# Kernel tuning notes

Hardware: AMD Instinct MI355X
Metric: run time of the kernel (lower is better)

The kernel has to match this reference:

```python
import jax, jax.numpy as jnp
import numpy as np

NUM_HEADS = 8
HEAD_SPLITS = [2, 3, 3]   # heads per conv window group (windows 3,5,7)


def _dwconv(x, w, b):
    # depthwise conv2d, SAME padding; x [B,Cg,H,W], w [Cg,1,k,k]
    k = w.shape[-1]
    pad = k // 2
    out = jax.lax.conv_general_dilated(
        x, w, window_strides=(1, 1), padding=[(pad, pad), (pad, pad)],
        feature_group_count=x.shape[1])
    return out + b[None, :, None, None]


def setup_inputs() -> dict:
    key = jax.random.key(0)
    ks = jax.random.split(key, 8)
    B, Hs, Ws, C = 16, 56, 56, 512
    N = 1 + Hs * Ws
    Ch = C // NUM_HEADS
    inp = {
        "x": jax.random.normal(ks[0], (B, N, C), dtype=jnp.float32),
        "qkv_w": jax.random.normal(ks[1], (3 * C, C), dtype=jnp.float32) * 0.02,
        "qkv_b": jnp.zeros((3 * C,), dtype=jnp.float32),
        "proj_w": jax.random.normal(ks[2], (C, C), dtype=jnp.float32) * 0.02,
        "proj_b": jnp.zeros((C,), dtype=jnp.float32),
        "conv_w3": jax.random.normal(ks[3], (2 * Ch, 1, 3, 3), dtype=jnp.float32) * 0.1,
        "conv_b3": jnp.zeros((2 * Ch,), dtype=jnp.float32),
        "conv_w5": jax.random.normal(ks[4], (3 * Ch, 1, 5, 5), dtype=jnp.float32) * 0.1,
        "conv_b5": jnp.zeros((3 * Ch,), dtype=jnp.float32),
        "conv_w7": jax.random.normal(ks[5], (3 * Ch, 1, 7, 7), dtype=jnp.float32) * 0.1,
        "conv_b7": jnp.zeros((3 * Ch,), dtype=jnp.float32),
        "H": 56,
        "W": 56,
    }
    return inp


def reference(x, qkv_w, qkv_b, proj_w, proj_b,
              conv_w3, conv_b3, conv_w5, conv_b5, conv_w7, conv_b7, H, W):
    B, N, C = x.shape
    h = NUM_HEADS
    Ch = C // h
    scale = Ch ** -0.5

    # qkv projection -> [3, B, h, N, Ch]
    qkv = (x @ qkv_w.T + qkv_b).reshape(B, N, 3, h, Ch)
    qkv = jnp.transpose(qkv, (2, 0, 3, 1, 4))
    q, k, v = qkv[0], qkv[1], qkv[2]

    # linear-attention factorization: softmax over tokens, then small Ch x Ch matmuls
    k_sm = jax.nn.softmax(k, axis=2)                     # softmax over N
    kv = jnp.einsum('bhnk,bhnd->bhkd', k_sm, v)          # [B,h,Ch,Ch]
    factor_att = jnp.einsum('bhnk,bhkd->bhnd', q, kv)    # [B,h,N,Ch]

    # conv relative-position encoding (CoaT ConvRelPosEnc)
    q_img = q[:, :, 1:, :]                               # drop CLS token
    v_img = v[:, :, 1:, :]
    v_img = jnp.transpose(v_img, (0, 1, 3, 2)).reshape(B, h * Ch, H, W)
    splits = np.cumsum([s * Ch for s in HEAD_SPLITS])[:-1]
    p3, p5, p7 = jnp.split(v_img, splits, axis=1)
    conv_v = jnp.concatenate([
        _dwconv(p3, conv_w3, conv_b3),
        _dwconv(p5, conv_w5, conv_b5),
        _dwconv(p7, conv_w7, conv_b7)], axis=1)           # [B,h*Ch,H,W]
    conv_v = jnp.transpose(conv_v.reshape(B, h, Ch, H * W), (0, 1, 3, 2))
    ev = q_img * conv_v                                   # [B,h,HW,Ch]
    crpe = jnp.concatenate(
        [jnp.zeros((B, h, 1, Ch), dtype=x.dtype), ev], axis=2)

    out = scale * factor_att + crpe                       # [B,h,N,Ch]
    out = jnp.transpose(out, (0, 2, 1, 3)).reshape(B, N, C)
    return out @ proj_w.T + proj_b
```

## Files before the change

### kernel.cpp

```cpp
#include <hip/hip_runtime.h>
#include <stdint.h>

#define NHEADS 8
#define NTOK   3137
#define BATCH  16
#define CDIM   512
#define MT     (BATCH*NTOK)

typedef unsigned short u16;
typedef float f32x4  __attribute__((ext_vector_type(4)));
typedef short bf16x8 __attribute__((ext_vector_type(8)));

__device__ __forceinline__ float bf2f(u16 u){
  union { uint32_t i; float f; } x; x.i = ((uint32_t)u) << 16; return x.f;
}
__device__ __forceinline__ u16 f2bf(float f){
  union { float f; uint32_t i; } x; x.f = f;
  uint32_t r = x.i + 0x7fffu + ((x.i >> 16) & 1u);
  return (u16)(r >> 16);
}
__device__ __forceinline__ void async_ld16(void* lds, const void* g){
  __builtin_amdgcn_global_load_lds((const __attribute__((address_space(1))) void*)g,
                                   (__attribute__((address_space(3))) void*)lds, 16, 0, 0);
}
#define BARM()   asm volatile("s_barrier" ::: "memory")
#define WAITV(N) asm volatile("s_waitcnt vmcnt(" #N ")" ::: "memory")
#define MFMA16(d,a,b) d = __builtin_amdgcn_mfma_f32_16x16x32_bf16(a,b,d,0,0,0)

__global__ void cvt_kernel(const float* __restrict__ src, u16* __restrict__ dst, int n4){
  int i = blockIdx.x * blockDim.x + threadIdx.x;
  if (i < n4){
    float4 v = ((const float4*)src)[i];
    uint32_t lo = ((uint32_t)f2bf(v.y) << 16) | f2bf(v.x);
    uint32_t hi = ((uint32_t)f2bf(v.w) << 16) | f2bf(v.z);
    ((uint2*)dst)[i] = make_uint2(lo, hi);
  }
}

template<int BM,int BN,int WM,int WN,int MODE>
__global__ __launch_bounds__(WM*WN*64, 2) void gemm2(
    const u16* __restrict__ A, const u16* __restrict__ Bw, const float* __restrict__ bias,
    u16* __restrict__ q_s, u16* __restrict__ k_s, u16* __restrict__ v_s,
    float* __restrict__ outF, int M)
{
  constexpr int THREADS = WM*WN*64;
  constexpr int MF = BM/(WM*16);
  constexpr int NF = BN/(WN*16);
  constexpr int WROWS = BM/WM;
  constexpr int WCOLS = BN/WN;
  static_assert((BM*8)/THREADS + (BN*8)/THREADS == 8, "vmcnt literal assumes 8 loads/stage");
  __shared__ __align__(16) u16 smem[2*(BM+BN)*64];

  const int t = threadIdx.x;
  const int w = t >> 6, l = t & 63;
  const int wr = w / WN, wc = w % WN;
  const int lr = l & 15, lg = l >> 4;

  const int nx = gridDim.x;
  const int nwg = nx * gridDim.y;
  const int orig = blockIdx.y * nx + blockIdx.x;
  const int q8 = nwg >> 3, r8 = nwg & 7;
  const int xcd = orig & 7;
  const int wgid = (xcd < r8 ? xcd*(q8+1) : r8*(q8+1) + (xcd-r8)*q8) + (orig >> 3);
  const int n0 = (wgid % nx) * BN;
  const int m0 = (wgid / nx) * BM;

  f32x4 acc[MF][NF];
#pragma unroll
  for (int i=0;i<MF;i++)
#pragma unroll
    for (int j=0;j<NF;j++) acc[i][j] = (f32x4){0.f,0.f,0.f,0.f};

  auto stage = [&](int bi, int k0){
    u16* da = smem + bi*(BM*64);
    u16* db = smem + 2*BM*64 + bi*(BN*64);
#pragma unroll
    for (int j=0;j<(BM*8)/THREADS;j++){
      int qc = t + THREADS*j;
      int R = qc >> 3, c = qc & 7;
      int cs = (c ^ (R & 7)) * 8;
      int ar = m0 + R; if (ar > M-1) ar = M-1;
      async_ld16(&da[qc*8], &A[(size_t)ar*512 + k0 + cs]);
    }
#pragma unroll
    for (int j=0;j<(BN*8)/THREADS;j++){
      int qc = t + THREADS*j;
      int R = qc >> 3, c = qc & 7;
      int cs = (c ^ (R & 7)) * 8;
      async_ld16(&db[qc*8], &Bw[(size_t)(n0+R)*512 + k0 + cs]);
    }
  };

  stage(0, 0);
  int cur = 0;
  for (int kt = 0; kt < 8; ++kt){
    if (kt < 7) stage(cur ^ 1, (kt+1)*64);
    if (kt < 7) { WAITV(8); } else { WAITV(0); }
    BARM();
    const u16* a_base = smem + cur*(BM*64);
    const u16* b_base = smem + 2*BM*64 + cur*(BN*64);
    __builtin_amdgcn_s_setprio(1);
#pragma unroll
    for (int ks=0; ks<2; ks++){
      bf16x8 af[MF], bfv[NF];
      int chunk = ks*4 + lg;
#pragma unroll
      for (int fi=0;fi<MF;fi++){
        int row = wr*WROWS + fi*16 + lr;
        af[fi] = *(const bf16x8*)&a_base[row*64 + ((chunk ^ (row & 7))*8)];
      }
#pragma unroll
      for (int fj=0;fj<NF;fj++){
        int col = wc*WCOLS + fj*16 + lr;
        bfv[fj] = *(const bf16x8*)&b_base[col*64 + ((chunk ^ (col & 7))*8)];
      }
#pragma unroll
      for (int fi=0;fi<MF;fi++)
#pragma unroll
        for (int fj=0;fj<NF;fj++)
          acc[fi][fj] = __builtin_amdgcn_mfma_f32_16x16x32_bf16(af[fi], bfv[fj], acc[fi][fj], 0, 0, 0);
    }
    __builtin_amdgcn_s_setprio(0);
    BARM();
    cur ^= 1;
  }

  if (MODE == 0){
    u16* warea = smem + w * (WROWS*WCOLS);
    float bvv[NF];
#pragma unroll
    for (int fj=0;fj<NF;fj++) bvv[fj] = bias[n0 + wc*WCOLS + fj*16 + lr];
#pragma unroll
    for (int fi=0;fi<MF;fi++)
#pragma unroll
      for (int fj=0;fj<NF;fj++)
#pragma unroll
        for (int r=0;r<4;r++)
          warea[(fi*16 + lg*4 + r)*WCOLS + fj*16 + lr] = f2bf(acc[fi][fj][r] + bvv[fj]);
    __syncthreads();
    const int colo = n0 + wc*WCOLS;
    const int part = colo >> 9;
    const int hq   = (colo >> 6) & 7;
    u16* dst = (part == 0) ? q_s : ((part == 1) ? k_s : v_s);
    const int rsub = l >> 3;
    const int csub = (l & 7) * 8;
#pragma unroll
    for (int pass=0; pass<WROWS/8; ++pass){
      int rl = pass*8 + rsub;
      int m = m0 + wr*WROWS + rl;
      if (m < M){
        int bb = m / NTOK;
        int n  = m - bb*NTOK;
        uint4 vv = *(const uint4*)&warea[rl*WCOLS + csub];
        *(uint4*)&dst[((size_t)(bb*8 + hq)*NTOK + n)*64 + csub] = vv;
      }
    }
  } else {
    float* warea = (float*)smem + w * (WROWS*WCOLS);
    float bvv[NF];
#pragma unroll
    for (int fj=0;fj<NF;fj++) bvv[fj] = bias[n0 + wc*WCOLS + fj*16 + lr];
#pragma unroll
    for (int fi=0;fi<MF;fi++)
#pragma unroll
      for (int fj=0;fj<NF;fj++)
#pragma unroll
        for (int r=0;r<4;r++)
          warea[(fi*16 + lg*4 + r)*WCOLS + fj*16 + lr] = acc[fi][fj][r] + bvv[fj];
    __syncthreads();
    const int colo = n0 + wc*WCOLS;
    const int rsub = l >> 4;
    const int csub = (l & 15) * 4;
#pragma unroll
    for (int pass=0; pass<WROWS/4; ++pass){
      int rl = pass*4 + rsub;
      int m = m0 + wr*WROWS + rl;
      if (m < M){
        float4 vv = *(const float4*)&warea[rl*WCOLS + csub];
        *(float4*)&outF[(size_t)m*512 + colo + csub] = vv;
      }
    }
  }
}

__global__ __launch_bounds__(256) void kv_partial(
    const u16* __restrict__ k_s, const u16* __restrict__ v_s,
    float* __restrict__ kv_p, float* __restrict__ s_p)
{
  __shared__ float smem[18432];
  const int t  = threadIdx.x;
  const int bh = blockIdx.x;
  const int hf = blockIdx.y;
  const size_t base = (size_t)bh * NTOK * 64;
  const int srow = t >> 3;
  const int scol = (t & 7) * 8;
  const int ns = t >> 6;
  const int kg = (t >> 3) & 7;
  const int dg = t & 7;

  float accv[8][8];
#pragma unroll
  for (int a=0;a<8;a++)
#pragma unroll
    for (int c=0;c<8;c++) accv[a][c] = 0.f;
  float s_loc[8];
#pragma unroll
  for (int i=0;i<8;i++) s_loc[i] = 0.f;

  float* ek = smem;
  float* vv = smem + 2048;
  const int n_beg = hf * 800;
  const int n_end = (hf == 3) ? NTOK : (n_beg + 800);

  for (int n0 = n_beg; n0 < n_end; n0 += 32){
    __syncthreads();
    int n = n0 + srow;
    float et[8], vf[8];
    if (n < n_end){
      uint4 kvec = *(const uint4*)&k_s[base + (size_t)n*64 + scol];
      uint4 vvec = *(const uint4*)&v_s[base + (size_t)n*64 + scol];
      const u16* kp = (const u16*)&kvec;
      const u16* vp = (const u16*)&vvec;
#pragma unroll
      for (int i=0;i<8;i++){
        et[i] = __expf(bf2f(kp[i]));
        s_loc[i] += et[i];
        vf[i] = bf2f(vp[i]);
      }
    } else {
#pragma unroll
      for (int i=0;i<8;i++){ et[i]=0.f; vf[i]=0.f; }
    }
    *(float4*)&ek[srow*64 + scol]     = make_float4(et[0],et[1],et[2],et[3]);
    *(float4*)&ek[srow*64 + scol + 4] = make_float4(et[4],et[5],et[6],et[7]);
    *(float4*)&vv[srow*64 + scol]     = make_float4(vf[0],vf[1],vf[2],vf[3]);
    *(float4*)&vv[srow*64 + scol + 4] = make_float4(vf[4],vf[5],vf[6],vf[7]);
    __syncthreads();
#pragma unroll
    for (int i=0;i<8;i++){
      int nl = ns + 4*i;
      float4 e0 = *(const float4*)&ek[nl*64 + kg*8];
      float4 e1 = *(const float4*)&ek[nl*64 + kg*8 + 4];
      float4 v0 = *(const float4*)&vv[nl*64 + dg*8];
      float4 v1 = *(const float4*)&vv[nl*64 + dg*8 + 4];
      float ea[8] = {e0.x,e0.y,e0.z,e0.w,e1.x,e1.y,e1.z,e1.w};
      float va[8] = {v0.x,v0.y,v0.z,v0.w,v1.x,v1.y,v1.z,v1.w};
#pragma unroll
      for (int a=0;a<8;a++)
#pragma unroll
        for (int c=0;c<8;c++) accv[a][c] += ea[a]*va[c];
    }
  }
  __syncthreads();
  float* part_kv = smem;
  float* part_s  = smem + 16384;
#pragma unroll
  for (int a=0;a<8;a++)
#pragma unroll
    for (int c=0;c<8;c++)
      part_kv[(size_t)ns*4096 + (kg*8+a)*64 + dg*8+c] = accv[a][c];
#pragma unroll
  for (int i=0;i<8;i++) part_s[srow*64 + scol + i] = s_loc[i];
  __syncthreads();
  const size_t obase = ((size_t)hf*128 + bh) * 4096;
  for (int i=0;i<16;i++){
    int e = t*16 + i;
    kv_p[obase + e] = part_kv[e] + part_kv[4096+e] + part_kv[8192+e] + part_kv[12288+e];
  }
  if (t < 64){
    float s = 0.f;
    for (int r=0;r<32;r++) s += part_s[r*64 + t];
    s_p[((size_t)hf*128 + bh)*64 + t] = s;
  }
}

__global__ void kv_reduce(const float* __restrict__ kv_p, const float* __restrict__ s_p,
                          u16* __restrict__ kvT){
  const int bh = blockIdx.x, t = threadIdx.x;
  for (int i=0;i<16;i++){
    int e = t*16 + i;
    int k = e >> 6, d = e & 63;
    float v = 0.f, S = 0.f;
#pragma unroll
    for (int hf=0; hf<4; hf++){
      v += kv_p[(size_t)(hf*128 + bh)*4096 + e];
      S += s_p[(hf*128 + bh)*64 + k];
    }
    kvT[(size_t)bh*4096 + d*64 + k] = f2bf(v / S);
  }
}

template<int R>
__global__ __launch_bounds__(256) void conv_fa(
    const u16* __restrict__ v_s, const u16* __restrict__ q_s,
    const u16* __restrict__ kvT,
    const float* __restrict__ wsrc, const float* __restrict__ bsrc,
    int h0, u16* __restrict__ out_pre)
{
  constexpr int KK = 2*R + 1;
  constexpr int TAPS = KK*KK;
  __shared__ __align__(16) u16 smem[8192 + KK*3584];
  u16* vt = smem + 8192;
  const int t = threadIdx.x;
  const int y  = blockIdx.x;
  const int hh = blockIdx.y;
  const int b  = blockIdx.z;
  const int h  = h0 + hh;
  const int bh = b*8 + h;
  const size_t base = (size_t)bh * NTOK * 64;
  const int n0 = 1 + y*56;

#pragma unroll
  for (int j=0;j<2;j++){
    int qq = t + 256*j;
    int row = qq >> 3, c = qq & 7;
    int cs = (c ^ (row & 7)) * 8;
    int n = n0 + row; if (n > NTOK-1) n = NTOK-1;
    async_ld16(&smem[qq*8], &q_s[base + (size_t)n*64 + cs]);
    async_ld16(&smem[4096 + qq*8], &kvT[(size_t)bh*4096 + row*64 + cs]);
  }
  for (int ry=0; ry<KK; ry++){
    int yy = y - R + ry;
    for (int idx = t; idx < 448; idx += 256){
      uint4 val = make_uint4(0u,0u,0u,0u);
      if (yy >= 0 && yy < 56)
        val = *(const uint4*)&v_s[base + (size_t)(1 + yy*56)*64 + idx*8];
      *(uint4*)&vt[ry*3584 + idx*8] = val;
    }
  }
  __syncthreads();

  const int w = t >> 6, l = t & 63;
  const int lr = l & 15, lg = l >> 4;
  f32x4 fac[4];
#pragma unroll
  for (int j=0;j<4;j++) fac[j] = (f32x4){0.f,0.f,0.f,0.f};
#pragma unroll
  for (int ks=0; ks<2; ks++){
    int chunk = ks*4 + lg;
    int arow = w*16 + lr;
    bf16x8 af = *(const bf16x8*)&smem[arow*64 + ((chunk ^ (arow & 7))*8)];
#pragma unroll
    for (int fj=0; fj<4; fj++){
      int col = fj*16 + lr;
      bf16x8 bvv = *(const bf16x8*)&smem[4096 + col*64 + ((chunk ^ (col & 7))*8)];
      MFMA16(fac[fj], af, bvv);
    }
  }

  const int d = l;
  const int xg = w;
  float wreg[TAPS];
#pragma unroll
  for (int i=0;i<TAPS;i++) wreg[i] = wsrc[(hh*64 + d)*TAPS + i];
  const float bias = bsrc[hh*64 + d];
  float creg[14];
#pragma unroll
  for (int i=0;i<14;i++) creg[i] = bias;
  const int x0 = xg * 14;
#pragma unroll
  for (int ry=0; ry<KK; ry++){
    float rw[14 + 2*R];
#pragma unroll
    for (int i=0; i<14+2*R; i++){
      int xx = x0 - R + i;
      rw[i] = (xx >= 0 && xx < 56) ? bf2f(vt[ry*3584 + xx*64 + d]) : 0.f;
    }
#pragma unroll
    for (int xi=0; xi<14; xi++)
#pragma unroll
      for (int rx=0; rx<KK; rx++)
        creg[xi] += rw[xi+rx] * wreg[ry*KK + rx];
  }

  float qv[14];
#pragma unroll
  for (int xi=0; xi<14; xi++){
    int row = x0 + xi;
    int chunk = d >> 3, e = d & 7;
    qv[xi] = bf2f(smem[row*64 + ((chunk ^ (row & 7))*8) + e]);
  }

  __syncthreads();
  float* fa = (float*)smem;
#pragma unroll
  for (int fj=0; fj<4; fj++)
#pragma unroll
    for (int r=0; r<4; r++)
      fa[(w*16 + lg*4 + r)*64 + fj*16 + lr] = 0.125f * fac[fj][r];
  __syncthreads();

#pragma unroll
  for (int xi=0; xi<14; xi++){
    int nn = n0 + x0 + xi;
    out_pre[((size_t)b*NTOK + nn)*CDIM + h*64 + d] =
        f2bf(fa[(x0 + xi)*64 + d] + creg[xi]*qv[xi]);
  }
}

__global__ void fa0_kernel(const u16* __restrict__ q_s, const u16* __restrict__ kvT,
                           u16* __restrict__ out_pre){
  const int b = blockIdx.x, t = threadIdx.x;
  const int h = t >> 6, d = t & 63;
  const int bh = b*8 + h;
  float s = 0.f;
#pragma unroll
  for (int k=0; k<64; k++)
    s += bf2f(q_s[(size_t)bh*NTOK*64 + k]) * bf2f(kvT[(size_t)bh*4096 + d*64 + k]);
  out_pre[(size_t)b*NTOK*CDIM + h*64 + d] = f2bf(0.125f * s);
}

extern "C" void kernel_launch(void* const* d_in, const int* in_sizes, int n_in,
                              void* d_out, int out_size, void* d_ws, size_t ws_size,
                              hipStream_t stream)
{
  const float* x      = (const float*)d_in[0];
  const float* qkv_w  = (const float*)d_in[1];
  const float* qkv_b  = (const float*)d_in[2];
  const float* proj_w = (const float*)d_in[3];
  const float* proj_b = (const float*)d_in[4];
  const float* w3 = (const float*)d_in[5];
  const float* b3 = (const float*)d_in[6];
  const float* w5 = (const float*)d_in[7];
  const float* b5 = (const float*)d_in[8];
  const float* w7 = (const float*)d_in[9];
  const float* b7 = (const float*)d_in[10];
  float* out = (float*)d_out;

  char* ws = (char*)d_ws;
  size_t off = 0;
  auto alloc = [&](size_t bytes) -> void* {
    void* p = ws + off;
    off += (bytes + 255) & ~(size_t)255;
    return p;
  };
  u16*   x_bf     = (u16*)alloc((size_t)MT*512*2);
  u16*   qkvw_bf  = (u16*)alloc((size_t)1536*512*2);
  u16*   projw_bf = (u16*)alloc((size_t)512*512*2);
  u16*   q_s      = (u16*)alloc((size_t)128*NTOK*64*2);
  u16*   k_s      = (u16*)alloc((size_t)128*NTOK*64*2);
  u16*   v_s      = (u16*)alloc((size_t)128*NTOK*64*2);
  u16*   kvT      = (u16*)alloc((size_t)128*4096*2);
  float* kv_p     = (float*)alloc((size_t)4*128*4096*4);
  float* s_p      = (float*)alloc((size_t)4*128*64*4);
  u16*   out_pre  = x_bf;

  { int n4 = (MT*512)/4;   cvt_kernel<<<(n4+255)/256, 256, 0, stream>>>(x, x_bf, n4); }
  { int n4 = (1536*512)/4; cvt_kernel<<<(n4+255)/256, 256, 0, stream>>>(qkv_w, qkvw_bf, n4); }
  { int n4 = (512*512)/4;  cvt_kernel<<<(n4+255)/256, 256, 0, stream>>>(proj_w, projw_bf, n4); }

  gemm2<256,256,2,4,0><<<dim3(6, 197), 512, 0, stream>>>(
      x_bf, qkvw_bf, qkv_b, q_s, k_s, v_s, nullptr, MT);

  kv_partial<<<dim3(128, 4), 256, 0, stream>>>(k_s, v_s, kv_p, s_p);
  kv_reduce<<<128, 256, 0, stream>>>(kv_p, s_p, kvT);
  fa0_kernel<<<16, 512, 0, stream>>>(q_s, kvT, out_pre);

  conv_fa<1><<<dim3(56, 2, 16), 256, 0, stream>>>(v_s, q_s, kvT, w3, b3, 0, out_pre);
  conv_fa<2><<<dim3(56, 3, 16), 256, 0, stream>>>(v_s, q_s, kvT, w5, b5, 2, out_pre);
  conv_fa<3><<<dim3(56, 3, 16), 256, 0, stream>>>(v_s, q_s, kvT, w7, b7, 5, out_pre);

  gemm2<128,128,2,2,1><<<dim3(4, 393), 256, 0, stream>>>(
      out_pre, projw_bf, proj_b, nullptr, nullptr, nullptr, out, MT);
}
```

Before: 383.9 us.

## Use MFMA for KV reduction and unify proj GEMM to 256x256 tiles

Replaces the scalar FP32 outer-product kv_partial kernel with an MFMA-based kernel that stores exp(k) and v transposed in bf16 shared memory with XOR swizzle. It also fixes the GEMM template to 256x256 tiles for both the QKV and output projections, splitting the fp32 epilogue into two halves to fit shared memory. The explicit vmcnt waits and raw barriers are replaced by __syncthreads. The intent is to cut the FP32 ALU cost of the kv reduction and use larger proj tiles, at the price of bf16 rounding of exp(k) and possibly weaker load/compute overlap in the GEMM loop.

```diff
diff --git a/kernel.cpp b/kernel.cpp
--- a/kernel.cpp
+++ b/kernel.cpp
@@ -23,8 +23,6 @@
   __builtin_amdgcn_global_load_lds((const __attribute__((address_space(1))) void*)g,
                                    (__attribute__((address_space(3))) void*)lds, 16, 0, 0);
 }
-#define BARM()   asm volatile("s_barrier" ::: "memory")
-#define WAITV(N) asm volatile("s_waitcnt vmcnt(" #N ")" ::: "memory")
 #define MFMA16(d,a,b) d = __builtin_amdgcn_mfma_f32_16x16x32_bf16(a,b,d,0,0,0)
 
 __global__ void cvt_kernel(const float* __restrict__ src, u16* __restrict__ dst, int n4){
@@ -37,18 +35,16 @@
   }
 }
 
-template<int BM,int BN,int WM,int WN,int MODE>
-__global__ __launch_bounds__(WM*WN*64, 2) void gemm2(
+template<int MODE>
+__global__ __launch_bounds__(512, 2) void gemm2(
     const u16* __restrict__ A, const u16* __restrict__ Bw, const float* __restrict__ bias,
     u16* __restrict__ q_s, u16* __restrict__ k_s, u16* __restrict__ v_s,
     float* __restrict__ outF, int M)
 {
-  constexpr int THREADS = WM*WN*64;
-  constexpr int MF = BM/(WM*16);
-  constexpr int NF = BN/(WN*16);
-  constexpr int WROWS = BM/WM;
-  constexpr int WCOLS = BN/WN;
-  static_assert((BM*8)/THREADS + (BN*8)/THREADS == 8, "vmcnt literal assumes 8 loads/stage");
+  constexpr int BM=256, BN=256, WN=4;
+  constexpr int THREADS = 512;
+  constexpr int MF = 8, NF = 4;
+  constexpr int WROWS = 128, WCOLS = 64;
   __shared__ __align__(16) u16 smem[2*(BM+BN)*64];
 
   const int t = threadIdx.x;
@@ -92,11 +88,10 @@
   };
 
   stage(0, 0);
+  __syncthreads();
   int cur = 0;
   for (int kt = 0; kt < 8; ++kt){
     if (kt < 7) stage(cur ^ 1, (kt+1)*64);
-    if (kt < 7) { WAITV(8); } else { WAITV(0); }
-    BARM();
     const u16* a_base = smem + cur*(BM*64);
     const u16* b_base = smem + 2*BM*64 + cur*(BN*64);
     __builtin_amdgcn_s_setprio(1);
@@ -121,15 +116,16 @@
           acc[fi][fj] = __builtin_amdgcn_mfma_f32_16x16x32_bf16(af[fi], bfv[fj], acc[fi][fj], 0, 0, 0);
     }
     __builtin_amdgcn_s_setprio(0);
-    BARM();
+    __syncthreads();
     cur ^= 1;
   }
+
+  float bvv[NF];
+#pragma unroll
+  for (int fj=0;fj<NF;fj++) bvv[fj] = bias[n0 + wc*WCOLS + fj*16 + lr];
 
   if (MODE == 0){
     u16* warea = smem + w * (WROWS*WCOLS);
-    float bvv[NF];
-#pragma unroll
-    for (int fj=0;fj<NF;fj++) bvv[fj] = bias[n0 + wc*WCOLS + fj*16 + lr];
 #pragma unroll
     for (int fi=0;fi<MF;fi++)
 #pragma unroll
@@ -156,121 +152,117 @@
       }
     }
   } else {
-    float* warea = (float*)smem + w * (WROWS*WCOLS);
-    float bvv[NF];
-#pragma unroll
-    for (int fj=0;fj<NF;fj++) bvv[fj] = bias[n0 + wc*WCOLS + fj*16 + lr];
-#pragma unroll
-    for (int fi=0;fi<MF;fi++)
-#pragma unroll
-      for (int fj=0;fj<NF;fj++)
-#pragma unroll
-        for (int r=0;r<4;r++)
-          warea[(fi*16 + lg*4 + r)*WCOLS + fj*16 + lr] = acc[fi][fj][r] + bvv[fj];
-    __syncthreads();
+    constexpr int PR = WROWS/2;
+    float* warea = (float*)smem + w * (PR*WCOLS);
     const int colo = n0 + wc*WCOLS;
     const int rsub = l >> 4;
     const int csub = (l & 15) * 4;
 #pragma unroll
-    for (int pass=0; pass<WROWS/4; ++pass){
-      int rl = pass*4 + rsub;
-      int m = m0 + wr*WROWS + rl;
-      if (m < M){
-        float4 vv = *(const float4*)&warea[rl*WCOLS + csub];
-        *(float4*)&outF[(size_t)m*512 + colo + csub] = vv;
-      }
-    }
-  }
-}
-
-__global__ __launch_bounds__(256) void kv_partial(
+    for (int p=0; p<2; ++p){
+#pragma unroll
+      for (int fh=0; fh<MF/2; fh++){
+        int fi = p*(MF/2) + fh;
+#pragma unroll
+        for (int fj=0;fj<NF;fj++)
+#pragma unroll
+          for (int r=0;r<4;r++)
+            warea[(fh*16 + lg*4 + r)*WCOLS + fj*16 + lr] = acc[fi][fj][r] + bvv[fj];
+      }
+#pragma unroll
+      for (int pass=0; pass<PR/4; ++pass){
+        int rl = pass*4 + rsub;
+        int m = m0 + wr*WROWS + p*PR + rl;
+        if (m < M){
+          float4 vv = *(const float4*)&warea[rl*WCOLS + csub];
+          *(float4*)&outF[(size_t)m*512 + colo + csub] = vv;
+        }
+      }
+    }
+  }
+}
+
+__global__ __launch_bounds__(256) void kv_mfma(
     const u16* __restrict__ k_s, const u16* __restrict__ v_s,
     float* __restrict__ kv_p, float* __restrict__ s_p)
 {
-  __shared__ float smem[18432];
+  __shared__ __align__(16) u16 ekT[64*64];
+  __shared__ __align__(16) u16 vT[64*64];
+  __shared__ float part_s[32*64];
   const int t  = threadIdx.x;
   const int bh = blockIdx.x;
-  const int hf = blockIdx.y;
+  const int qq = blockIdx.y;
   const size_t base = (size_t)bh * NTOK * 64;
-  const int srow = t >> 3;
-  const int scol = (t & 7) * 8;
-  const int ns = t >> 6;
-  const int kg = (t >> 3) & 7;
-  const int dg = t & 7;
-
-  float accv[8][8];
-#pragma unroll
-  for (int a=0;a<8;a++)
-#pragma unroll
-    for (int c=0;c<8;c++) accv[a][c] = 0.f;
+  const int c_beg = (qq==0) ? 0 : (qq==1) ? 13 : (qq==2) ? 26 : 39;
+  const int c_end = (qq==3) ? 50 : (c_beg + 13);
+  const int w = t >> 6, l = t & 63;
+  const int lr = l & 15, lg = l >> 4;
+  const int nl0 = t >> 3;
+  const int dc  = (t & 7) * 8;
+
+  f32x4 acc[4];
+#pragma unroll
+  for (int j=0;j<4;j++) acc[j] = (f32x4){0.f,0.f,0.f,0.f};
   float s_loc[8];
 #pragma unroll
   for (int i=0;i<8;i++) s_loc[i] = 0.f;
 
-  float* ek = smem;
-  float* vv = smem + 2048;
-  const int n_beg = hf * 800;
-  const int n_end = (hf == 3) ? NTOK : (n_beg + 800);
-
-  for (int n0 = n_beg; n0 < n_end; n0 += 32){
+  for (int ch = c_beg; ch < c_end; ++ch){
+    const int n0c = ch*64;
     __syncthreads();
-    int n = n0 + srow;
-    float et[8], vf[8];
-    if (n < n_end){
-      uint4 kvec = *(const uint4*)&k_s[base + (size_t)n*64 + scol];
-      uint4 vvec = *(const uint4*)&v_s[base + (size_t)n*64 + scol];
+#pragma unroll
+    for (int half=0; half<2; ++half){
+      int nloc = nl0 + half*32;
+      int n = n0c + nloc;
+      bool valid = (n < NTOK);
+      uint4 kvec = make_uint4(0u,0u,0u,0u), vvec = make_uint4(0u,0u,0u,0u);
+      if (valid){
+        kvec = *(const uint4*)&k_s[base + (size_t)n*64 + dc];
+        vvec = *(const uint4*)&v_s[base + (size_t)n*64 + dc];
+      }
       const u16* kp = (const u16*)&kvec;
       const u16* vp = (const u16*)&vvec;
+      const int nc = nloc >> 3, ne = nloc & 7;
 #pragma unroll
       for (int i=0;i<8;i++){
-        et[i] = __expf(bf2f(kp[i]));
-        s_loc[i] += et[i];
-        vf[i] = bf2f(vp[i]);
-      }
-    } else {
-#pragma unroll
-      for (int i=0;i<8;i++){ et[i]=0.f; vf[i]=0.f; }
-    }
-    *(float4*)&ek[srow*64 + scol]     = make_float4(et[0],et[1],et[2],et[3]);
-    *(float4*)&ek[srow*64 + scol + 4] = make_float4(et[4],et[5],et[6],et[7]);
-    *(float4*)&vv[srow*64 + scol]     = make_float4(vf[0],vf[1],vf[2],vf[3]);
-    *(float4*)&vv[srow*64 + scol + 4] = make_float4(vf[4],vf[5],vf[6],vf[7]);
+        float e = valid ? __expf(bf2f(kp[i])) : 0.f;
+        s_loc[i] += e;
+        int row = dc + i;
+        int pos = row*64 + ((nc ^ (row & 7) ^ ((row >> 3) & 7))*8) + ne;
+        ekT[pos] = f2bf(e);
+        vT[pos]  = valid ? vp[i] : (u16)0;
+      }
+    }
     __syncthreads();
-#pragma unroll
-    for (int i=0;i<8;i++){
-      int nl = ns + 4*i;
-      float4 e0 = *(const float4*)&ek[nl*64 + kg*8];
-      float4 e1 = *(const float4*)&ek[nl*64 + kg*8 + 4];
-      float4 v0 = *(const float4*)&vv[nl*64 + dg*8];
-      float4 v1 = *(const float4*)&vv[nl*64 + dg*8 + 4];
-      float ea[8] = {e0.x,e0.y,e0.z,e0.w,e1.x,e1.y,e1.z,e1.w};
-      float va[8] = {v0.x,v0.y,v0.z,v0.w,v1.x,v1.y,v1.z,v1.w};
-#pragma unroll
-      for (int a=0;a<8;a++)
-#pragma unroll
-        for (int c=0;c<8;c++) accv[a][c] += ea[a]*va[c];
-    }
-  }
+    __builtin_amdgcn_s_setprio(1);
+#pragma unroll
+    for (int ks=0; ks<2; ks++){
+      int chnk = ks*4 + lg;
+      int arow = w*16 + lr;
+      bf16x8 af = *(const bf16x8*)&ekT[arow*64 + ((chnk ^ (arow & 7) ^ ((arow >> 3) & 7))*8)];
+#pragma unroll
+      for (int fj=0; fj<4; fj++){
+        int col = fj*16 + lr;
+        bf16x8 bv = *(const bf16x8*)&vT[col*64 + ((chnk ^ (col & 7) ^ ((col >> 3) & 7))*8)];
+        MFMA16(acc[fj], af, bv);
+      }
+    }
+    __builtin_amdgcn_s_setprio(0);
+  }
+
+  const size_t obase = ((size_t)qq*128 + bh) * 4096;
+#pragma unroll
+  for (int fj=0; fj<4; fj++)
+#pragma unroll
+    for (int r=0; r<4; r++)
+      kv_p[obase + (size_t)(w*16 + lg*4 + r)*64 + fj*16 + lr] = acc[fj][r];
+
+#pragma unroll
+  for (int i=0;i<8;i++) part_s[nl0*64 + dc + i] = s_loc[i];
   __syncthreads();
-  float* part_kv = smem;
-  float* part_s  = smem + 16384;
-#pragma unroll
-  for (int a=0;a<8;a++)
-#pragma unroll
-    for (int c=0;c<8;c++)
-      part_kv[(size_t)ns*4096 + (kg*8+a)*64 + dg*8+c] = accv[a][c];
-#pragma unroll
-  for (int i=0;i<8;i++) part_s[srow*64 + scol + i] = s_loc[i];
-  __syncthreads();
-  const size_t obase = ((size_t)hf*128 + bh) * 4096;
-  for (int i=0;i<16;i++){
-    int e = t*16 + i;
-    kv_p[obase + e] = part_kv[e] + part_kv[4096+e] + part_kv[8192+e] + part_kv[12288+e];
-  }
   if (t < 64){
     float s = 0.f;
     for (int r=0;r<32;r++) s += part_s[r*64 + t];
-    s_p[((size_t)hf*128 + bh)*64 + t] = s;
+    s_p[((size_t)qq*128 + bh)*64 + t] = s;
   }
 }
 
@@ -449,10 +441,9 @@
   { int n4 = (1536*512)/4; cvt_kernel<<<(n4+255)/256, 256, 0, stream>>>(qkv_w, qkvw_bf, n4); }
   { int n4 = (512*512)/4;  cvt_kernel<<<(n4+255)/256, 256, 0, stream>>>(proj_w, projw_bf, n4); }
 
-  gemm2<256,256,2,4,0><<<dim3(6, 197), 512, 0, stream>>>(
-      x_bf, qkvw_bf, qkv_b, q_s, k_s, v_s, nullptr, MT);
-
-  kv_partial<<<dim3(128, 4), 256, 0, stream>>>(k_s, v_s, kv_p, s_p);
+  gemm2<0><<<dim3(6, 197), 512, 0, stream>>>(x_bf, qkvw_bf, qkv_b, q_s, k_s, v_s, nullptr, MT);
+
+  kv_mfma<<<dim3(128, 4), 256, 0, stream>>>(k_s, v_s, kv_p, s_p);
   kv_reduce<<<128, 256, 0, stream>>>(kv_p, s_p, kvT);
   fa0_kernel<<<16, 512, 0, stream>>>(q_s, kvT, out_pre);
 
@@ -460,6 +451,5 @@
   conv_fa<2><<<dim3(56, 3, 16), 256, 0, stream>>>(v_s, q_s, kvT, w5, b5, 2, out_pre);
   conv_fa<3><<<dim3(56, 3, 16), 256, 0, stream>>>(v_s, q_s, kvT, w7, b7, 5, out_pre);
 
-  gemm2<128,128,2,2,1><<<dim3(4, 393), 256, 0, stream>>>(
-      out_pre, projw_bf, proj_b, nullptr, nullptr, nullptr, out, MT);
-}
+  gemm2<1><<<dim3(2, 197), 512, 0, stream>>>(out_pre, projw_bf, proj_b, nullptr, nullptr, nullptr, out, MT);
+}
```

After: 351.7 us. 8.4% less time.
